# Optimization experiments

Measured on AMD Instinct MI355X. Metric: run time of the kernel, lower is better.

The kernel has to match this reference:

```python
import jax, jax.numpy as jnp
import numpy as np

SINKHORN_ALPHA = 20.0
WEIGHT_LOSS_ECR = 100.0
OT_MAX_ITER = 100
STOP_THR = 0.005
EPS = 1e-16


def setup_inputs() -> dict:
    key = jax.random.key(0)
    # cost matrix: [num_topics, vocab]
    M = jax.random.uniform(key, (512, 65536), dtype=jnp.float32)
    return {"M": M}


def reference(M) -> jnp.ndarray:
    n, m = M.shape
    a = jnp.full((n, 1), 1.0 / n, dtype=M.dtype)   # row marginal
    b = jnp.full((m, 1), 1.0 / m, dtype=M.dtype)   # col marginal
    u0 = jnp.full((n, 1), 1.0 / n, dtype=M.dtype)
    K = jnp.exp(-M * SINKHORN_ALPHA)               # [n, m]

    def cond_fn(carry):
        u, v, err, cpt = carry
        return (err > STOP_THR) & (cpt < OT_MAX_ITER)

    def body_fn(carry):
        u, v, err, cpt = carry
        v = b / (K.T @ u + EPS)                    # [m, 1]
        u = a / (K @ v + EPS)                      # [n, 1]
        cpt = cpt + 1
        # convergence check every 50 iters (cpt % 50 == 1), matching torch loop
        err = jax.lax.cond(
            cpt % 50 == 1,
            lambda: jnp.sum(jnp.abs(v * (K.T @ u) - b)).astype(err.dtype),
            lambda: err,
        )
        return (u, v, err, cpt)

    init = (u0, jnp.zeros((m, 1), dtype=M.dtype), jnp.asarray(1.0, M.dtype), jnp.asarray(0, jnp.int32))
    u, v, _, _ = jax.lax.while_loop(cond_fn, body_fn, init)

    transp = u * (K * v.T)                         # [n, m] transport plan
    loss_ECR = jnp.sum(transp * M) * WEIGHT_LOSS_ECR
    return loss_ECR
```

## Files before the change

kernel.cpp:

```cpp
#include <hip/hip_runtime.h>

#define NROW 512
#define NCOL 65536

static __device__ __forceinline__ float wave_sum(float x) {
  #pragma unroll
  for (int off = 32; off; off >>= 1) x += __shfl_down(x, off, 64);
  return x;
}

static __device__ __forceinline__ void gbar(int* cnt, int* phase) {
  __syncthreads();
  if (threadIdx.x == 0) {
    int ph = atomicAdd(phase, 0);
    __threadfence();
    if (atomicAdd(cnt, 1) == (int)gridDim.x - 1) {
      atomicExch(cnt, 0);
      __threadfence();
      atomicAdd(phase, 1);
    } else {
      while (atomicAdd(phase, 0) == ph) { __builtin_amdgcn_s_sleep(8); }
    }
    __threadfence();
  }
  __syncthreads();
}

__global__ __launch_bounds__(512)
void k1a_colsum(const float* __restrict__ M, float* __restrict__ tPart,
                float* __restrict__ eA, int* __restrict__ bar) {
  const int tid = threadIdx.x, bid = blockIdx.x;
  const int colblk = bid & 511, band = bid >> 9;
  const int chunk = tid & 31;
  const int part  = tid >> 5;
  const int col0  = (colblk << 7) + (chunk << 2);
  const int r0    = (band << 8) + (part << 4);

  __shared__ float sCol[16 * 128];

  if (bid == 0 && tid < 8) eA[tid] = 0.f;
  if (bid == 0 && tid < 2) bar[tid] = 0;

  const float* Mp = M + (size_t)r0 * NCOL + col0;
  float4 cs = {0.f, 0.f, 0.f, 0.f};
  #pragma unroll 8
  for (int rr = 0; rr < 16; ++rr) {
    float4 m = *(const float4*)(Mp + (size_t)rr * NCOL);
    cs.x += __expf(-20.f * m.x);
    cs.y += __expf(-20.f * m.y);
    cs.z += __expf(-20.f * m.z);
    cs.w += __expf(-20.f * m.w);
  }
  *(float4*)(sCol + part * 128 + (chunk << 2)) = cs;
  __syncthreads();
  if (tid < 128) {
    float t = 0.f;
    #pragma unroll
    for (int p = 0; p < 16; ++p) t += sCol[p * 128 + tid];
    tPart[(size_t)band * NCOL + (colblk << 7) + tid] = t;
  }
}

__global__ __launch_bounds__(256)
void k1b_v1(const float* __restrict__ tPart, float* __restrict__ v) {
  const int gid = blockIdx.x * 256 + threadIdx.x;
  const int col0 = gid << 2;
  const float am = 1.0f / NROW, bm = 1.0f / NCOL, EPSV = 1e-16f;
  float4 p0 = *(const float4*)(tPart + col0);
  float4 p1 = *(const float4*)(tPart + NCOL + col0);
  float4 vv = {bm / ((p0.x + p1.x) * am + EPSV),
               bm / ((p0.y + p1.y) * am + EPSV),
               bm / ((p0.z + p1.z) * am + EPSV),
               bm / ((p0.w + p1.w) * am + EPSV)};
  *(float4*)(v + col0) = vv;
}

__global__ __launch_bounds__(1024)
void k2_rowdot(const float* __restrict__ M, const float* __restrict__ v,
               float* __restrict__ u) {
  const int tid = threadIdx.x, row = blockIdx.x;
  const float am = 1.0f / NROW, EPSV = 1e-16f;
  const float4* M4 = (const float4*)M + (size_t)row * (NCOL / 4);
  const float4* V4 = (const float4*)v;
  __shared__ float sRed[16];

  float acc = 0.f;
  #pragma unroll 4
  for (int it = 0; it < NCOL / 4 / 1024; ++it) {
    const int c = (it << 10) + tid;
    float4 m = M4[c];
    float4 vv = V4[c];
    acc += __expf(-20.f * m.x) * vv.x + __expf(-20.f * m.y) * vv.y
         + __expf(-20.f * m.z) * vv.z + __expf(-20.f * m.w) * vv.w;
  }
  acc = wave_sum(acc);
  if ((tid & 63) == 0) sRed[tid >> 6] = acc;
  __syncthreads();
  if (tid == 0) {
    float s = 0.f;
    #pragma unroll
    for (int w = 0; w < 16; ++w) s += sRed[w];
    u[row] = am / (s + EPSV);
  }
}

__global__ __launch_bounds__(512)
void k3a_colsum_u(const float* __restrict__ M, const float* __restrict__ v,
                  const float* __restrict__ u, float* __restrict__ tPart,
                  float* __restrict__ eA) {
  const int tid = threadIdx.x, bid = blockIdx.x;
  const int colblk = bid & 511, band = bid >> 9;
  const int chunk = tid & 31;
  const int part  = tid >> 5;
  const int col0  = (colblk << 7) + (chunk << 2);
  const int r0l   = part << 4;

  __shared__ float sU[256];
  __shared__ float sCol[16 * 128];
  __shared__ float sRed[8];

  if (tid < 256) sU[tid] = u[(band << 8) + tid];
  __syncthreads();

  const float4 vv = *(const float4*)(v + col0);
  const float* Mp = M + (size_t)((band << 8) + r0l) * NCOL + col0;
  float4 cs = {0.f, 0.f, 0.f, 0.f};
  float lacc = 0.f;
  #pragma unroll 8
  for (int rr = 0; rr < 16; ++rr) {
    float4 m = *(const float4*)(Mp + (size_t)rr * NCOL);
    float e0 = __expf(-20.f * m.x), e1 = __expf(-20.f * m.y);
    float e2 = __expf(-20.f * m.z), e3 = __expf(-20.f * m.w);
    float us = sU[r0l + rr];
    cs.x = fmaf(e0, us, cs.x);
    cs.y = fmaf(e1, us, cs.y);
    cs.z = fmaf(e2, us, cs.z);
    cs.w = fmaf(e3, us, cs.w);
    lacc += us * (e0 * m.x * vv.x + e1 * m.y * vv.y
                + e2 * m.z * vv.z + e3 * m.w * vv.w);
  }
  *(float4*)(sCol + part * 128 + (chunk << 2)) = cs;
  lacc = wave_sum(lacc);
  if ((tid & 63) == 0) sRed[tid >> 6] = lacc;
  __syncthreads();
  if (tid < 128) {
    float t = 0.f;
    #pragma unroll
    for (int p = 0; p < 16; ++p) t += sCol[p * 128 + tid];
    tPart[(size_t)band * NCOL + (colblk << 7) + tid] = t;
  }
  if (tid == 0)
    atomicAdd(&eA[2], sRed[0] + sRed[1] + sRed[2] + sRed[3]
                    + sRed[4] + sRed[5] + sRed[6] + sRed[7]);
}

__global__ __launch_bounds__(256)
void k3b_err(const float* __restrict__ tPart, const float* __restrict__ v,
             float* __restrict__ tArr, float* __restrict__ eA,
             float* __restrict__ out, int* __restrict__ done) {
  const int tid = threadIdx.x;
  const int gid = blockIdx.x * 256 + tid;
  const int col0 = gid << 2;
  const float bm = 1.0f / NCOL;
  __shared__ float sRed[4];

  float4 p0 = *(const float4*)(tPart + col0);
  float4 p1 = *(const float4*)(tPart + NCOL + col0);
  float4 t = {p0.x + p1.x, p0.y + p1.y, p0.z + p1.z, p0.w + p1.w};
  *(float4*)(tArr + col0) = t;
  float4 vv = *(const float4*)(v + col0);
  float pe = fabsf(vv.x * t.x - bm) + fabsf(vv.y * t.y - bm)
           + fabsf(vv.z * t.z - bm) + fabsf(vv.w * t.w - bm);
  pe = wave_sum(pe);
  if ((tid & 63) == 0) sRed[tid >> 6] = pe;
  __syncthreads();
  if (tid == 0) {
    atomicAdd(&eA[0], sRed[0] + sRed[1] + sRed[2] + sRed[3]);
    __threadfence();
    int old = atomicAdd((int*)(eA + 4), 1);
    if (old == (int)gridDim.x - 1) {
      __threadfence();
      float err = atomicAdd(&eA[0], 0.f);
      float ls  = atomicAdd(&eA[2], 0.f);
      if (err <= 0.005f) { out[0] = 100.f * ls; done[0] = 1; }
      else               { out[0] = 0.f;        done[0] = 0; }
    }
  }
}

__global__ __launch_bounds__(1024)
void k5_fallback(const float* __restrict__ M, float* __restrict__ out,
                 float* __restrict__ v, float* __restrict__ u,
                 const float* __restrict__ tArr, float* __restrict__ eA,
                 const int* __restrict__ done, int* __restrict__ bar) {
  if (done[0]) return;
  const int tid = threadIdx.x, bid = blockIdx.x;
  const float am = 1.0f / NROW, bm = 1.0f / NCOL, EPSV = 1e-16f;
  int* cnt = bar;
  int* phs = bar + 1;

  __shared__ float sU[NROW];
  __shared__ float sCol[16 * 256];
  __shared__ float sRedA[16], sRedB[16];
  __shared__ float sErr;

  const int chunk = tid & 63;
  const int part  = tid >> 6;
  const int col0  = (bid << 8) + (chunk << 2);
  const int r0    = part << 5;
  const int row0  = bid << 1;

  float tt = (tid < 256) ? tArr[(bid << 8) + tid] : 0.f;

  int cpt = 1;
  while (true) {
    if (tid < 256) v[(bid << 8) + tid] = bm / (tt + EPSV);
    gbar(cnt, phs);
    cpt++;

    {
      const float4* M40 = (const float4*)M + (size_t)row0 * (NCOL / 4);
      const float4* M41 = (const float4*)M + (size_t)(row0 + 1) * (NCOL / 4);
      const float4* V4  = (const float4*)v;
      float ra = 0.f, rb = 0.f;
      #pragma unroll 4
      for (int it = 0; it < NCOL / 4 / 1024; ++it) {
        const int c = (it << 10) + tid;
        float4 vv = V4[c];
        float4 m0 = M40[c], m1 = M41[c];
        ra += __expf(-20.f * m0.x) * vv.x + __expf(-20.f * m0.y) * vv.y
            + __expf(-20.f * m0.z) * vv.z + __expf(-20.f * m0.w) * vv.w;
        rb += __expf(-20.f * m1.x) * vv.x + __expf(-20.f * m1.y) * vv.y
            + __expf(-20.f * m1.z) * vv.z + __expf(-20.f * m1.w) * vv.w;
      }
      ra = wave_sum(ra); rb = wave_sum(rb);
      if ((tid & 63) == 0) { sRedA[tid >> 6] = ra; sRedB[tid >> 6] = rb; }
      __syncthreads();
      if (tid < 2) {
        const float* sr = (tid == 0) ? sRedA : sRedB;
        float s = 0.f;
        #pragma unroll
        for (int w = 0; w < 16; ++w) s += sr[w];
        u[row0 + tid] = am / (s + EPSV);
      }
    }
    gbar(cnt, phs);
    if (cpt >= 100) break;

    if (tid < NROW) sU[tid] = u[tid];
    __syncthreads();
    float4 cs = {0.f, 0.f, 0.f, 0.f};
    #pragma unroll 4
    for (int r = r0; r < r0 + 32; ++r) {
      float4 m = *(const float4*)(M + (size_t)r * NCOL + col0);
      float us = sU[r];
      cs.x = fmaf(__expf(-20.f * m.x), us, cs.x);
      cs.y = fmaf(__expf(-20.f * m.y), us, cs.y);
      cs.z = fmaf(__expf(-20.f * m.z), us, cs.z);
      cs.w = fmaf(__expf(-20.f * m.w), us, cs.w);
    }
    *(float4*)(sCol + part * 256 + (chunk << 2)) = cs;
    __syncthreads();
    if (tid < 256) {
      tt = 0.f;
      #pragma unroll
      for (int p = 0; p < 16; ++p) tt += sCol[p * 256 + tid];
    }

    if (cpt == 51) {
      float pe = (tid < 256) ? fabsf(v[(bid << 8) + tid] * tt - bm) : 0.f;
      pe = wave_sum(pe);
      __syncthreads();
      if ((tid & 63) == 0) sRedA[tid >> 6] = pe;
      __syncthreads();
      if (tid == 0) {
        float s = 0.f;
        #pragma unroll
        for (int w = 0; w < 16; ++w) s += sRedA[w];
        atomicAdd(&eA[1], s);
      }
      gbar(cnt, phs);
      if (tid == 0) sErr = atomicAdd(&eA[1], 0.f);
      __syncthreads();
      if (sErr <= 0.005f) break;
    }
  }

  __syncthreads();
  if (tid < NROW) sU[tid] = u[tid];
  __syncthreads();
  {
    const float4 vv = *(const float4*)(v + col0);
    float lacc = 0.f;
    #pragma unroll 4
    for (int r = r0; r < r0 + 32; ++r) {
      float4 m = *(const float4*)(M + (size_t)r * NCOL + col0);
      float us = sU[r];
      lacc += us * (__expf(-20.f * m.x) * m.x * vv.x
                  + __expf(-20.f * m.y) * m.y * vv.y
                  + __expf(-20.f * m.z) * m.z * vv.z
                  + __expf(-20.f * m.w) * m.w * vv.w);
    }
    lacc = wave_sum(lacc);
    if ((tid & 63) == 0) sRedA[tid >> 6] = lacc;
    __syncthreads();
    if (tid == 0) {
      float s = 0.f;
      #pragma unroll
      for (int w = 0; w < 16; ++w) s += sRedA[w];
      atomicAdd(out, 100.f * s);
    }
  }
}

extern "C" void kernel_launch(void* const* d_in, const int* in_sizes, int n_in,
                              void* d_out, int out_size, void* d_ws, size_t ws_size,
                              hipStream_t stream) {
  const float* M = (const float*)d_in[0];
  float* out = (float*)d_out;

  const size_t offV = 0;
  const size_t offT = offV + (size_t)NCOL * sizeof(float);
  const size_t offU = offT + (size_t)NCOL * sizeof(float);
  const size_t offE = offU + 4096;
  const size_t offD = offE + 256;
  const size_t offB = offD + 256;
  const size_t offP = offB + 256;
  const size_t need = offP + 2 * (size_t)NCOL * sizeof(float);
  if (ws_size < need) return;

  char* ws = (char*)d_ws;
  float* v     = (float*)(ws + offV);
  float* tArr  = (float*)(ws + offT);
  float* u     = (float*)(ws + offU);
  float* eA    = (float*)(ws + offE);
  int*   done  = (int*)(ws + offD);
  int*   bar   = (int*)(ws + offB);
  float* tPart = (float*)(ws + offP);

  k1a_colsum  <<<dim3(1024), dim3(512),  0, stream>>>(M, tPart, eA, bar);
  k1b_v1      <<<dim3(64),   dim3(256),  0, stream>>>(tPart, v);
  k2_rowdot   <<<dim3(512),  dim3(1024), 0, stream>>>(M, v, u);
  k3a_colsum_u<<<dim3(1024), dim3(512),  0, stream>>>(M, v, u, tPart, eA);
  k3b_err     <<<dim3(64),   dim3(256),  0, stream>>>(tPart, v, tArr, eA, out, done);
  k5_fallback <<<dim3(256),  dim3(1024), 0, stream>>>(M, out, v, u, tArr, eA,
                                                      done, bar);
}
```

Measured before the change: 243.3 us.

## Cache exp(-20M) as bf16 in workspace and reuse it in later passes

The first column-sum pass now also writes K = exp(-20*M) to a bf16 copy in workspace. The row-dot and the weighted column-sum passes read that half-size array instead of re-reading fp32 M and recomputing exp. The loss term rebuilds M as -log(K)/20 from the bf16 value. This trades one extra 64 MB write for halved reads in two later passes. It also lowers the precision of K and of the reconstructed M, and adds a log per element. The column-block and band split changes to 4 bands of 128 rows, so the partial-sum reductions now add 4 bands.

```diff
diff --git a/kernel.cpp b/kernel.cpp
--- a/kernel.cpp
+++ b/kernel.cpp
@@ -2,6 +2,7 @@
 
 #define NROW 512
 #define NCOL 65536
+#define BANDS 4
 
 static __device__ __forceinline__ float wave_sum(float x) {
   #pragma unroll
@@ -26,38 +27,55 @@
   __syncthreads();
 }
 
+static __device__ __forceinline__ unsigned short f2bf(float f) {
+  unsigned int u = __float_as_uint(f);
+  u += 0x7FFFu + ((u >> 16) & 1u);
+  return (unsigned short)(u >> 16);
+}
+static __device__ __forceinline__ float bf2f_lo(unsigned int w) {
+  return __uint_as_float(w << 16);
+}
+static __device__ __forceinline__ float bf2f_hi(unsigned int w) {
+  return __uint_as_float(w & 0xFFFF0000u);
+}
+
 __global__ __launch_bounds__(512)
-void k1a_colsum(const float* __restrict__ M, float* __restrict__ tPart,
-                float* __restrict__ eA, int* __restrict__ bar) {
+void k1a_colsum(const float* __restrict__ M, unsigned short* __restrict__ E16,
+                float* __restrict__ tPart, float* __restrict__ eA,
+                int* __restrict__ bar) {
   const int tid = threadIdx.x, bid = blockIdx.x;
-  const int colblk = bid & 511, band = bid >> 9;
-  const int chunk = tid & 31;
-  const int part  = tid >> 5;
-  const int col0  = (colblk << 7) + (chunk << 2);
-  const int r0    = (band << 8) + (part << 4);
-
-  __shared__ float sCol[16 * 128];
+  const int colblk = bid & 255, band = bid >> 8;
+  const int chunk = tid & 63;
+  const int part  = tid >> 6;
+  const int col0  = (colblk << 8) + (chunk << 2);
+  const int r0    = (band << 7) + (part << 4);
+
+  __shared__ float sCol[8 * 256];
 
   if (bid == 0 && tid < 8) eA[tid] = 0.f;
   if (bid == 0 && tid < 2) bar[tid] = 0;
 
   const float* Mp = M + (size_t)r0 * NCOL + col0;
+  unsigned short* Ep = E16 + (size_t)r0 * NCOL + col0;
   float4 cs = {0.f, 0.f, 0.f, 0.f};
   #pragma unroll 8
   for (int rr = 0; rr < 16; ++rr) {
     float4 m = *(const float4*)(Mp + (size_t)rr * NCOL);
-    cs.x += __expf(-20.f * m.x);
-    cs.y += __expf(-20.f * m.y);
-    cs.z += __expf(-20.f * m.z);
-    cs.w += __expf(-20.f * m.w);
-  }
-  *(float4*)(sCol + part * 128 + (chunk << 2)) = cs;
-  __syncthreads();
-  if (tid < 128) {
+    float e0 = __expf(-20.f * m.x), e1 = __expf(-20.f * m.y);
+    float e2 = __expf(-20.f * m.z), e3 = __expf(-20.f * m.w);
+    cs.x += e0; cs.y += e1; cs.z += e2; cs.w += e3;
+    uint2 w;
+    w.x = (unsigned int)f2bf(e0) | ((unsigned int)f2bf(e1) << 16);
+    w.y = (unsigned int)f2bf(e2) | ((unsigned int)f2bf(e3) << 16);
+    *(uint2*)(Ep + (size_t)rr * NCOL) = w;
+  }
+  *(float4*)(sCol + part * 256 + (chunk << 2)) = cs;
+  __syncthreads();
+  if (tid < 256) {
     float t = 0.f;
     #pragma unroll
-    for (int p = 0; p < 16; ++p) t += sCol[p * 128 + tid];
-    tPart[(size_t)band * NCOL + (colblk << 7) + tid] = t;
+    for (int p = 0; p < 8; ++p) t += sCol[p * 256 + tid];
+    tPart[(size_t)band * NCOL + (colblk << 8) + tid] = t;
   }
 }
 
@@ -66,32 +84,36 @@
   const int gid = blockIdx.x * 256 + threadIdx.x;
   const int col0 = gid << 2;
   const float am = 1.0f / NROW, bm = 1.0f / NCOL, EPSV = 1e-16f;
-  float4 p0 = *(const float4*)(tPart + col0);
-  float4 p1 = *(const float4*)(tPart + NCOL + col0);
-  float4 vv = {bm / ((p0.x + p1.x) * am + EPSV),
-               bm / ((p0.y + p1.y) * am + EPSV),
-               bm / ((p0.z + p1.z) * am + EPSV),
-               bm / ((p0.w + p1.w) * am + EPSV)};
+  float4 t = {0.f, 0.f, 0.f, 0.f};
+  #pragma unroll
+  for (int b = 0; b < BANDS; ++b) {
+    float4 p = *(const float4*)(tPart + (size_t)b * NCOL + col0);
+    t.x += p.x; t.y += p.y; t.z += p.z; t.w += p.w;
+  }
+  float4 vv = {bm / (t.x * am + EPSV), bm / (t.y * am + EPSV),
+               bm / (t.z * am + EPSV), bm / (t.w * am + EPSV)};
   *(float4*)(v + col0) = vv;
 }
 
 __global__ __launch_bounds__(1024)
-void k2_rowdot(const float* __restrict__ M, const float* __restrict__ v,
-               float* __restrict__ u) {
+void k2_rowdot(const unsigned short* __restrict__ E16,
+               const float* __restrict__ v, float* __restrict__ u) {
   const int tid = threadIdx.x, row = blockIdx.x;
   const float am = 1.0f / NROW, EPSV = 1e-16f;
-  const float4* M4 = (const float4*)M + (size_t)row * (NCOL / 4);
+  const uint4* E4 = (const uint4*)(E16 + (size_t)row * NCOL);
   const float4* V4 = (const float4*)v;
   __shared__ float sRed[16];
 
   float acc = 0.f;
   #pragma unroll 4
-  for (int it = 0; it < NCOL / 4 / 1024; ++it) {
+  for (int it = 0; it < NCOL / 8 / 1024; ++it) {
     const int c = (it << 10) + tid;
-    float4 m = M4[c];
-    float4 vv = V4[c];
-    acc += __expf(-20.f * m.x) * vv.x + __expf(-20.f * m.y) * vv.y
-         + __expf(-20.f * m.z) * vv.z + __expf(-20.f * m.w) * vv.w;
+    uint4 w = E4[c];
+    float4 va = V4[2 * c], vb = V4[2 * c + 1];
+    acc += bf2f_lo(w.x) * va.x + bf2f_hi(w.x) * va.y
+         + bf2f_lo(w.y) * va.z + bf2f_hi(w.y) * va.w
+         + bf2f_lo(w.z) * vb.x + bf2f_hi(w.z) * vb.y
+         + bf2f_lo(w.w) * vb.z + bf2f_hi(w.w) * vb.w;
   }
   acc = wave_sum(acc);
   if ((tid & 63) == 0) sRed[tid >> 6] = acc;
@@ -105,49 +127,53 @@
 }
 
 __global__ __launch_bounds__(512)
-void k3a_colsum_u(const float* __restrict__ M, const float* __restrict__ v,
-                  const float* __restrict__ u, float* __restrict__ tPart,
-                  float* __restrict__ eA) {
+void k3a_colsum_u(const unsigned short* __restrict__ E16,
+                  const float* __restrict__ v, const float* __restrict__ u,
+                  float* __restrict__ tPart, float* __restrict__ eA) {
   const int tid = threadIdx.x, bid = blockIdx.x;
-  const int colblk = bid & 511, band = bid >> 9;
-  const int chunk = tid & 31;
-  const int part  = tid >> 5;
-  const int col0  = (colblk << 7) + (chunk << 2);
+  const int colblk = bid & 255, band = bid >> 8;
+  const int chunk = tid & 63;
+  const int part  = tid >> 6;
+  const int col0  = (colblk << 8) + (chunk << 2);
   const int r0l   = part << 4;
 
-  __shared__ float sU[256];
-  __shared__ float sCol[16 * 128];
+  __shared__ float sU[128];
+  __shared__ float sCol[8 * 256];
   __shared__ float sRed[8];
 
-  if (tid < 256) sU[tid] = u[(band << 8) + tid];
+  if (tid < 128) sU[tid] = u[(band << 7) + tid];
   __syncthreads();
 
   const float4 vv = *(const float4*)(v + col0);
-  const float* Mp = M + (size_t)((band << 8) + r0l) * NCOL + col0;
+  const unsigned short* Ep = E16 + (size_t)((band << 7) + r0l) * NCOL + col0;
   float4 cs = {0.f, 0.f, 0.f, 0.f};
   float lacc = 0.f;
   #pragma unroll 8
   for (int rr = 0; rr < 16; ++rr) {
-    float4 m = *(const float4*)(Mp + (size_t)rr * NCOL);
-    float e0 = __expf(-20.f * m.x), e1 = __expf(-20.f * m.y);
-    float e2 = __expf(-20.f * m.z), e3 = __expf(-20.f * m.w);
+    uint2 w = *(const uint2*)(Ep + (size_t)rr * NCOL);
+    float e0 = bf2f_lo(w.x), e1 = bf2f_hi(w.x);
+    float e2 = bf2f_lo(w.y), e3 = bf2f_hi(w.y);
     float us = sU[r0l + rr];
     cs.x = fmaf(e0, us, cs.x);
     cs.y = fmaf(e1, us, cs.y);
     cs.z = fmaf(e2, us, cs.z);
     cs.w = fmaf(e3, us, cs.w);
-    lacc += us * (e0 * m.x * vv.x + e1 * m.y * vv.y
-                + e2 * m.z * vv.z + e3 * m.w * vv.w);
-  }
-  *(float4*)(sCol + part * 128 + (chunk << 2)) = cs;
+    float m0 = __logf(e0) * (-0.05f);
+    float m1 = __logf(e1) * (-0.05f);
+    float m2 = __logf(e2) * (-0.05f);
+    float m3 = __logf(e3) * (-0.05f);
+    lacc += us * (e0 * m0 * vv.x + e1 * m1 * vv.y
+                + e2 * m2 * vv.z + e3 * m3 * vv.w);
+  }
+  *(float4*)(sCol + part * 256 + (chunk << 2)) = cs;
   lacc = wave_sum(lacc);
   if ((tid & 63) == 0) sRed[tid >> 6] = lacc;
   __syncthreads();
-  if (tid < 128) {
+  if (tid < 256) {
     float t = 0.f;
     #pragma unroll
-    for (int p = 0; p < 16; ++p) t += sCol[p * 128 + tid];
-    tPart[(size_t)band * NCOL + (colblk << 7) + tid] = t;
+    for (int p = 0; p < 8; ++p) t += sCol[p * 256 + tid];
+    tPart[(size_t)band * NCOL + (colblk << 8) + tid] = t;
   }
   if (tid == 0)
     atomicAdd(&eA[2], sRed[0] + sRed[1] + sRed[2] + sRed[3]
@@ -164,9 +190,12 @@
   const float bm = 1.0f / NCOL;
   __shared__ float sRed[4];
 
-  float4 p0 = *(const float4*)(tPart + col0);
-  float4 p1 = *(const float4*)(tPart + NCOL + col0);
-  float4 t = {p0.x + p1.x, p0.y + p1.y, p0.z + p1.z, p0.w + p1.w};
+  float4 t = {0.f, 0.f, 0.f, 0.f};
+  #pragma unroll
+  for (int b = 0; b < BANDS; ++b) {
+    float4 p = *(const float4*)(tPart + (size_t)b * NCOL + col0);
+    t.x += p.x; t.y += p.y; t.z += p.z; t.w += p.w;
+  }
   *(float4*)(tArr + col0) = t;
   float4 vv = *(const float4*)(v + col0);
   float pe = fabsf(vv.x * t.x - bm) + fabsf(vv.y * t.y - bm)
@@ -326,7 +355,8 @@
   const size_t offD = offE + 256;
   const size_t offB = offD + 256;
   const size_t offP = offB + 256;
-  const size_t need = offP + 2 * (size_t)NCOL * sizeof(float);
+  const size_t offE16 = offP + (size_t)BANDS * NCOL * sizeof(float);
+  const size_t need = offE16 + (size_t)NROW * NCOL * sizeof(unsigned short);
   if (ws_size < need) return;
 
   char* ws = (char*)d_ws;
@@ -337,11 +367,12 @@
   int*   done  = (int*)(ws + offD);
   int*   bar   = (int*)(ws + offB);
   float* tPart = (float*)(ws + offP);
-
-  k1a_colsum  <<<dim3(1024), dim3(512),  0, stream>>>(M, tPart, eA, bar);
+  unsigned short* E16 = (unsigned short*)(ws + offE16);
+
+  k1a_colsum  <<<dim3(1024), dim3(512),  0, stream>>>(M, E16, tPart, eA, bar);
   k1b_v1      <<<dim3(64),   dim3(256),  0, stream>>>(tPart, v);
-  k2_rowdot   <<<dim3(512),  dim3(1024), 0, stream>>>(M, v, u);
-  k3a_colsum_u<<<dim3(1024), dim3(512),  0, stream>>>(M, v, u, tPart, eA);
+  k2_rowdot   <<<dim3(512),  dim3(1024), 0, stream>>>(E16, v, u);
+  k3a_colsum_u<<<dim3(1024), dim3(512),  0, stream>>>(E16, v, u, tPart, eA);
   k3b_err     <<<dim3(64),   dim3(256),  0, stream>>>(tPart, v, tArr, eA, out, done);
   k5_fallback <<<dim3(256),  dim3(1024), 0, stream>>>(M, out, v, u, tArr, eA,
                                                       done, bar);
```

Result: no change. 243.0 us, median of 2 (-0.1%).
